# Kernel optimization log

Hardware: AMD Instinct MI355X
Metric: run time of the kernel (lower is better)

## Reference

```python
import jax, jax.numpy as jnp
import numpy as np

MARGIN = 1.0
EPS = 1e-8  # torch.cosine_similarity default eps


def _cosine(a, b):
    num = jnp.sum(a * b, axis=1)
    den = jnp.maximum(jnp.linalg.norm(a, axis=1) * jnp.linalg.norm(b, axis=1), EPS)
    return num / den


def setup_inputs() -> dict:
    key = jax.random.key(0)
    k1, k2 = jax.random.split(key)
    B, D = 8192, 512
    anchor = jax.random.normal(k1, (B, D), dtype=jnp.float32)
    positive = jax.random.normal(k2, (B, D), dtype=jnp.float32)
    return {"anchor": anchor, "positive": positive}


def reference(anchor, positive):
    B = positive.shape[0]
    a_n = anchor / jnp.linalg.norm(anchor, axis=1, keepdims=True)
    p_n = positive / jnp.linalg.norm(positive, axis=1, keepdims=True)
    sim = a_n @ p_n.T                      # [B, B] cosine similarity
    mask = 1.0 - jnp.eye(B, dtype=sim.dtype)
    sim = sim * mask                       # zero diagonal
    # margin branch of NegariveSampler (margin=1): abs(sim - margin), zeros -> -inf, argmax
    score = jnp.abs(sim - MARGIN) * mask
    score = jnp.where(score == 0.0, -jnp.inf, score)
    neg_idx = jnp.argmax(score, axis=1)    # [B]
    neg = p_n[neg_idx]                     # gather normalized positives as negatives
    cos_ap = _cosine(anchor, positive)
    cos_an = _cosine(anchor, neg)
    loss = jax.nn.relu(MARGIN + cos_ap - cos_an)
    return loss.mean()
```

## Files before the change

### kernel.cpp

```cpp
#include <hip/hip_runtime.h>
#include <stdint.h>

typedef int   i32x8 __attribute__((ext_vector_type(8)));
typedef float f32x4 __attribute__((ext_vector_type(4)));

#define B_ROWS 8192
#define D_DIM  512
#define BM 256
#define BN 256
#define BK 128
#define N_BLOCKS 1024

__device__ __forceinline__ uint32_t enc_f32(float f) {
  uint32_t s = __float_as_uint(f);
  return (s & 0x80000000u) ? ~s : (s | 0x80000000u);
}
__device__ __forceinline__ float dec_f32(uint32_t e) {
  uint32_t s = (e & 0x80000000u) ? (e ^ 0x80000000u) : ~e;
  return __uint_as_float(s);
}

__global__ __launch_bounds__(256) void norm_kernel(
    const float* __restrict__ anchor, const float* __restrict__ positive,
    uint32_t* __restrict__ a8, uint32_t* __restrict__ p8,
    float* __restrict__ cos_ap, uint32_t* __restrict__ minenc)
{
  const int wave = threadIdx.x >> 6, lane = threadIdx.x & 63;
  const int r = blockIdx.x * 4 + wave;

  const float4* av = (const float4*)(anchor   + (size_t)r * D_DIM) + lane * 2;
  const float4* pv = (const float4*)(positive + (size_t)r * D_DIM) + lane * 2;
  float4 a0 = av[0], a1 = av[1];
  float4 p0 = pv[0], p1 = pv[1];

  float sa = a0.x*a0.x + a0.y*a0.y + a0.z*a0.z + a0.w*a0.w
           + a1.x*a1.x + a1.y*a1.y + a1.z*a1.z + a1.w*a1.w;
  float sp = p0.x*p0.x + p0.y*p0.y + p0.z*p0.z + p0.w*p0.w
           + p1.x*p1.x + p1.y*p1.y + p1.z*p1.z + p1.w*p1.w;
  float dp = a0.x*p0.x + a0.y*p0.y + a0.z*p0.z + a0.w*p0.w
           + a1.x*p1.x + a1.y*p1.y + a1.z*p1.z + a1.w*p1.w;

#pragma unroll
  for (int d = 1; d < 64; d <<= 1) {
    sa += __shfl_xor(sa, d);
    sp += __shfl_xor(sp, d);
    dp += __shfl_xor(dp, d);
  }

  const float na = sqrtf(sa), np = sqrtf(sp);
  const float ia = 1.0f / na, ip = 1.0f / np;

  float na0 = a0.x*ia, na1 = a0.y*ia, na2 = a0.z*ia, na3 = a0.w*ia;
  float na4 = a1.x*ia, na5 = a1.y*ia, na6 = a1.z*ia, na7 = a1.w*ia;
  float np0 = p0.x*ip, np1 = p0.y*ip, np2 = p0.z*ip, np3 = p0.w*ip;
  float np4 = p1.x*ip, np5 = p1.y*ip, np6 = p1.z*ip, np7 = p1.w*ip;

  uint32_t aw0 = __builtin_amdgcn_cvt_pk_fp8_f32(na0, na1, 0,  false);
  aw0          = __builtin_amdgcn_cvt_pk_fp8_f32(na2, na3, aw0, true);
  uint32_t aw1 = __builtin_amdgcn_cvt_pk_fp8_f32(na4, na5, 0,  false);
  aw1          = __builtin_amdgcn_cvt_pk_fp8_f32(na6, na7, aw1, true);
  uint32_t pw0 = __builtin_amdgcn_cvt_pk_fp8_f32(np0, np1, 0,  false);
  pw0          = __builtin_amdgcn_cvt_pk_fp8_f32(np2, np3, pw0, true);
  uint32_t pw1 = __builtin_amdgcn_cvt_pk_fp8_f32(np4, np5, 0,  false);
  pw1          = __builtin_amdgcn_cvt_pk_fp8_f32(np6, np7, pw1, true);

  ((uint2*)a8)[(size_t)r * 64 + lane] = make_uint2(aw0, aw1);
  ((uint2*)p8)[(size_t)r * 64 + lane] = make_uint2(pw0, pw1);

  if (lane == 0) {
    cos_ap[r] = dp / fmaxf(na * np, 1e-8f);
    minenc[r] = 0xFFFFFFFFu;
  }
}

__device__ __forceinline__ void load16_to_lds(const void* g, void* l) {
  __builtin_amdgcn_global_load_lds(
      (__attribute__((address_space(1))) uint32_t*)(uintptr_t)(g),
      (__attribute__((address_space(3))) uint32_t*)(uintptr_t)(l),
      16, 0, 0);
}

__global__ __launch_bounds__(512, 2) void simmin_kernel(
    const uint8_t* __restrict__ a8, const uint8_t* __restrict__ p8,
    uint32_t* __restrict__ minenc)
{
  __shared__ __attribute__((aligned(16))) uint8_t Alds[2][BM * BK];
  __shared__ __attribute__((aligned(16))) uint8_t Plds[2][BN * BK];
  __shared__ float redmin[2][4][128];

  const int tid  = threadIdx.x;
  const int lane = tid & 63;
  const int wave = tid >> 6;
  const int waveM = wave >> 2;
  const int waveN = wave & 3;
  const int quad = lane >> 4;
  const int l15  = lane & 15;

  const int bid = blockIdx.x;
  const int blockRow = (bid & 7) * 4 + ((bid >> 3) & 3);
  const int blockCol = bid >> 5;

  f32x4 acc[8][4];
  const f32x4 zero = {0.f, 0.f, 0.f, 0.f};
#pragma unroll
  for (int i = 0; i < 8; i++)
#pragma unroll
    for (int j = 0; j < 4; j++) acc[i][j] = zero;

  const int srow = lane >> 3;
  const int sk   = (lane & 7) ^ srow;
  const uint8_t* aBase = a8 + (size_t)(blockRow * BM) * D_DIM;
  const uint8_t* pBase = p8 + (size_t)(blockCol * BN) * D_DIM;

  auto stage = [&](int k0, int buf) {
#pragma unroll
    for (int c = 0; c < 4; c++) {
      const int chunk = wave * 4 + c;
      const size_t goff = (size_t)(chunk * 8 + srow) * D_DIM + k0 + sk * 16;
      load16_to_lds(aBase + goff, &Alds[buf][chunk * 1024]);
      load16_to_lds(pBase + goff, &Plds[buf][chunk * 1024]);
    }
  };

  stage(0, 0);

#pragma unroll
  for (int k = 0; k < 4; k++) {
    const int buf = k & 1;
    __syncthreads();

    i32x8 bfr[4];
#pragma unroll
    for (int nf = 0; nf < 4; nf++) {
      const int r = waveN * 64 + nf * 16 + l15;
      const int rx = r & 7;
      const int4 lo = *(const int4*)&Plds[buf][r * BK + (((quad * 2 + 0) ^ rx) * 16)];
      const int4 hi = *(const int4*)&Plds[buf][r * BK + (((quad * 2 + 1) ^ rx) * 16)];
      bfr[nf] = (i32x8){lo.x, lo.y, lo.z, lo.w, hi.x, hi.y, hi.z, hi.w};
    }

    if (k < 3) stage((k + 1) * BK, buf ^ 1);

#pragma unroll
    for (int mf = 0; mf < 8; mf++) {
      const int r = waveM * 128 + mf * 16 + l15;
      const int rx = r & 7;
      const int4 lo = *(const int4*)&Alds[buf][r * BK + (((quad * 2 + 0) ^ rx) * 16)];
      const int4 hi = *(const int4*)&Alds[buf][r * BK + (((quad * 2 + 1) ^ rx) * 16)];
      const i32x8 af = (i32x8){lo.x, lo.y, lo.z, lo.w, hi.x, hi.y, hi.z, hi.w};
#pragma unroll
      for (int nf = 0; nf < 4; nf++)
        acc[mf][nf] = __builtin_amdgcn_mfma_scale_f32_16x16x128_f8f6f4(
            af, bfr[nf], acc[mf][nf],
            0, 0,
            0, 0x7F7F7F7F,
            0, 0x7F7F7F7F);
    }
  }

  const int rowTileBase = blockRow * BM + waveM * 128;
  const int colTileBase = blockCol * BN + waveN * 64;

  float rm[8][4];
#pragma unroll
  for (int mf = 0; mf < 8; mf++)
#pragma unroll
    for (int r = 0; r < 4; r++) rm[mf][r] = 3.0e38f;

#pragma unroll
  for (int mf = 0; mf < 8; mf++) {
#pragma unroll
    for (int nf = 0; nf < 4; nf++) {
      const int col = colTileBase + nf * 16 + l15;
#pragma unroll
      for (int r = 0; r < 4; r++) {
        const int row = rowTileBase + mf * 16 + quad * 4 + r;
        const float v = acc[mf][nf][r];
        rm[mf][r] = (row == col) ? rm[mf][r] : fminf(rm[mf][r], v);
      }
    }
  }
#pragma unroll
  for (int d = 1; d < 16; d <<= 1)
#pragma unroll
    for (int mf = 0; mf < 8; mf++)
#pragma unroll
      for (int r = 0; r < 4; r++)
        rm[mf][r] = fminf(rm[mf][r], __shfl_xor(rm[mf][r], d));

  if (l15 == 0) {
#pragma unroll
    for (int mf = 0; mf < 8; mf++)
#pragma unroll
      for (int r = 0; r < 4; r++)
        redmin[waveM][waveN][mf * 16 + quad * 4 + r] = rm[mf][r];
  }
  __syncthreads();

  if (tid < 256) {
    const int wm = tid >> 7, idx = tid & 127;
    const float m = fminf(fminf(redmin[wm][0][idx], redmin[wm][1][idx]),
                          fminf(redmin[wm][2][idx], redmin[wm][3][idx]));
    atomicMin(&minenc[blockRow * BM + tid], enc_f32(m));
  }
}

__global__ __launch_bounds__(1024) void finalize_kernel(
    const uint32_t* __restrict__ minenc, const float* __restrict__ cos_ap,
    float* __restrict__ out)
{
  float sum = 0.0f;
#pragma unroll
  for (int r = threadIdx.x; r < B_ROWS; r += 1024)
    sum += fmaxf(0.0f, 1.0f + cos_ap[r] - dec_f32(minenc[r]));

#pragma unroll
  for (int d = 1; d < 64; d <<= 1) sum += __shfl_xor(sum, d);
  __shared__ float s[16];
  if ((threadIdx.x & 63) == 0) s[threadIdx.x >> 6] = sum;
  __syncthreads();
  if (threadIdx.x < 64) {
    float t = (threadIdx.x < 16) ? s[threadIdx.x] : 0.0f;
#pragma unroll
    for (int d = 1; d < 16; d <<= 1) t += __shfl_xor(t, d);
    if (threadIdx.x == 0) out[0] = t * (1.0f / (float)B_ROWS);
  }
}

extern "C" void kernel_launch(void* const* d_in, const int* in_sizes, int n_in,
                              void* d_out, int out_size, void* d_ws, size_t ws_size,
                              hipStream_t stream) {
  const float* anchor   = (const float*)d_in[0];
  const float* positive = (const float*)d_in[1];

  char* ws = (char*)d_ws;
  uint32_t* a8     = (uint32_t*)(ws);
  uint32_t* p8     = (uint32_t*)(ws + (4ull << 20));
  float*    cos_ap = (float*)(ws + (8ull << 20));
  uint32_t* minenc = (uint32_t*)(ws + (8ull << 20) + (32ull << 10));
  float*    out = (float*)d_out;

  norm_kernel<<<B_ROWS / 4, 256, 0, stream>>>(anchor, positive, a8, p8,
                                              cos_ap, minenc);
  simmin_kernel<<<N_BLOCKS, 512, 0, stream>>>((const uint8_t*)a8,
                                              (const uint8_t*)p8, minenc);
  finalize_kernel<<<1, 1024, 0, stream>>>(minenc, cos_ap, out);
}
```

Baseline: 125.9 us.

## Restructure FP8 GEMM main loop into ping-pong phases with split staging

Replaces the simple double-buffered K loop with a phased schedule. Each K tile is split into four phases of two MFMA rows each, bracketed by explicit s_barrier, lgkmcnt waits, sched_barrier and s_setprio. Global-to-LDS staging is split into halves, and the first two K tiles are prefetched up front. The aim is to interleave LDS reads, async global loads and MFMA issue across waves so load latency is hidden and MFMA throughput stays high, at the cost of more barriers and hand-placed waitcnt logic that may be fragile.

```diff
diff --git a/kernel.cpp b/kernel.cpp
--- a/kernel.cpp
+++ b/kernel.cpp
@@ -112,51 +112,78 @@
   const uint8_t* aBase = a8 + (size_t)(blockRow * BM) * D_DIM;
   const uint8_t* pBase = p8 + (size_t)(blockCol * BN) * D_DIM;
 
-  auto stage = [&](int k0, int buf) {
-#pragma unroll
-    for (int c = 0; c < 4; c++) {
-      const int chunk = wave * 4 + c;
-      const size_t goff = (size_t)(chunk * 8 + srow) * D_DIM + k0 + sk * 16;
+  auto stage_half = [&](int t, int h, int buf) {
+#pragma unroll
+    for (int c = 0; c < 2; c++) {
+      const int chunk = h * 16 + wave * 2 + c;
+      const size_t goff = (size_t)(chunk * 8 + srow) * D_DIM + t * BK + sk * 16;
       load16_to_lds(aBase + goff, &Alds[buf][chunk * 1024]);
       load16_to_lds(pBase + goff, &Plds[buf][chunk * 1024]);
     }
   };
 
-  stage(0, 0);
-
-#pragma unroll
-  for (int k = 0; k < 4; k++) {
-    const int buf = k & 1;
-    __syncthreads();
+  auto read_af = [&](int buf, int mf) -> i32x8 {
+    const int r = waveM * 128 + mf * 16 + l15;
+    const int rx = r & 7;
+    const int4 lo = *(const int4*)&Alds[buf][r * BK + (((quad * 2 + 0) ^ rx) * 16)];
+    const int4 hi = *(const int4*)&Alds[buf][r * BK + (((quad * 2 + 1) ^ rx) * 16)];
+    return (i32x8){lo.x, lo.y, lo.z, lo.w, hi.x, hi.y, hi.z, hi.w};
+  };
+  auto read_bf = [&](int buf, int nf) -> i32x8 {
+    const int r = waveN * 64 + nf * 16 + l15;
+    const int rx = r & 7;
+    const int4 lo = *(const int4*)&Plds[buf][r * BK + (((quad * 2 + 0) ^ rx) * 16)];
+    const int4 hi = *(const int4*)&Plds[buf][r * BK + (((quad * 2 + 1) ^ rx) * 16)];
+    return (i32x8){lo.x, lo.y, lo.z, lo.w, hi.x, hi.y, hi.z, hi.w};
+  };
+
+#define MFMA_ROW(mf_, af_)                                                    \
+  _Pragma("unroll")                                                           \
+  for (int nf = 0; nf < 4; nf++)                                              \
+    acc[mf_][nf] = __builtin_amdgcn_mfma_scale_f32_16x16x128_f8f6f4(          \
+        af_, bfr[nf], acc[mf_][nf], 0, 0, 0, 0x7F7F7F7F, 0, 0x7F7F7F7F);
+
+#define PHASE(mfA, mfB, STAGE_STMT, TAIL_STMT)                                \
+  {                                                                           \
+    i32x8 afa = read_af(buf, (mfA));                                          \
+    i32x8 afb = read_af(buf, (mfB));                                          \
+    STAGE_STMT;                                                               \
+    __builtin_amdgcn_s_barrier();                                             \
+    asm volatile("s_waitcnt lgkmcnt(0)" ::: "memory");                        \
+    __builtin_amdgcn_sched_barrier(0);                                        \
+    __builtin_amdgcn_s_setprio(1);                                            \
+    MFMA_ROW((mfA), afa);                                                     \
+    MFMA_ROW((mfB), afb);                                                     \
+    __builtin_amdgcn_s_setprio(0);                                            \
+    TAIL_STMT;                                                                \
+    __builtin_amdgcn_s_barrier();                                             \
+  }
+
+  stage_half(0, 0, 0); stage_half(0, 1, 0);
+  stage_half(1, 0, 1); stage_half(1, 1, 1);
+  asm volatile("s_waitcnt vmcnt(8)" ::: "memory");
+  __builtin_amdgcn_s_barrier();
+
+#pragma unroll
+  for (int t = 0; t < 4; t++) {
+    const int buf = t & 1;
 
     i32x8 bfr[4];
 #pragma unroll
-    for (int nf = 0; nf < 4; nf++) {
-      const int r = waveN * 64 + nf * 16 + l15;
-      const int rx = r & 7;
-      const int4 lo = *(const int4*)&Plds[buf][r * BK + (((quad * 2 + 0) ^ rx) * 16)];
-      const int4 hi = *(const int4*)&Plds[buf][r * BK + (((quad * 2 + 1) ^ rx) * 16)];
-      bfr[nf] = (i32x8){lo.x, lo.y, lo.z, lo.w, hi.x, hi.y, hi.z, hi.w};
-    }
-
-    if (k < 3) stage((k + 1) * BK, buf ^ 1);
-
-#pragma unroll
-    for (int mf = 0; mf < 8; mf++) {
-      const int r = waveM * 128 + mf * 16 + l15;
-      const int rx = r & 7;
-      const int4 lo = *(const int4*)&Alds[buf][r * BK + (((quad * 2 + 0) ^ rx) * 16)];
-      const int4 hi = *(const int4*)&Alds[buf][r * BK + (((quad * 2 + 1) ^ rx) * 16)];
-      const i32x8 af = (i32x8){lo.x, lo.y, lo.z, lo.w, hi.x, hi.y, hi.z, hi.w};
-#pragma unroll
-      for (int nf = 0; nf < 4; nf++)
-        acc[mf][nf] = __builtin_amdgcn_mfma_scale_f32_16x16x128_f8f6f4(
-            af, bfr[nf], acc[mf][nf],
-            0, 0,
-            0, 0x7F7F7F7F,
-            0, 0x7F7F7F7F);
-    }
-  }
+    for (int nf = 0; nf < 4; nf++) bfr[nf] = read_bf(buf, nf);
+
+    PHASE(0, 1,
+          { if (t == 1) stage_half(2, 0, 0);  if (t == 2) stage_half(3, 0, 1); },
+          {});
+    PHASE(2, 3,
+          { if (t == 1) stage_half(2, 1, 0);  if (t == 2) stage_half(3, 1, 1); },
+          {});
+    PHASE(4, 5, {}, {});
+    PHASE(6, 7, {},
+          { if (t < 3) asm volatile("s_waitcnt vmcnt(0)" ::: "memory"); });
+  }
+#undef PHASE
+#undef MFMA_ROW
 
   const int rowTileBase = blockRow * BM + waveM * 128;
   const int colTileBase = blockCol * BN + waveN * 64;
```

Measured after the change: 125.2 us. No clear change (-0.5%).
